# Optimization experiments

Measured on AMD Instinct MI355X. Metric: run time of the kernel, lower is better.

The kernel has to match this reference:

```python
import jax, jax.numpy as jnp
import numpy as np

N = 100000
E = 1600000
H = 2
F_IN = 128
D = 64
DIAL = 256


def setup_inputs() -> dict:
    key = jax.random.key(0)
    ks = jax.random.split(key, 10)
    return {
        "entity_features": jax.random.normal(ks[0], (N, 1, F_IN), jnp.float32),
        "relation_features": jax.random.normal(ks[1], (E, 1, F_IN), jnp.float32),
        "dialogue_context": jax.random.normal(ks[2], (N, DIAL), jnp.float32),
        "w_m": jax.random.normal(ks[3], (H, F_IN, D), jnp.float32) * 0.05,
        "w_q": jax.random.normal(ks[4], (H, F_IN, D), jnp.float32) * 0.05,
        "w_k": jax.random.normal(ks[5], (H, F_IN, D), jnp.float32) * 0.05,
        "w_h_entity": jax.random.normal(ks[6], (H * D, D), jnp.float32) * 0.05,
        "w_h_dialogue": jax.random.normal(ks[7], (DIAL, D), jnp.float32) * 0.05,
        "src": jax.random.randint(ks[8], (E,), 0, N, jnp.int32),
        "dst": jax.random.randint(ks[9], (E,), 0, N, jnp.int32),
    }


def reference(entity_features, relation_features, dialogue_context,
              w_m, w_q, w_k, w_h_entity, w_h_dialogue, src, dst):
    n = entity_features.shape[0]
    h = w_m.shape[0]
    # broadcast single-head features across heads (torch .repeat(1, H, 1))
    f = jnp.broadcast_to(entity_features, (n, h, entity_features.shape[-1]))  # (N,H,F)
    r = jnp.broadcast_to(relation_features,
                         (relation_features.shape[0], h, relation_features.shape[-1]))  # (E,H,F)
    q = jnp.einsum('nhf,hfd->nhd', f, w_q)      # dst attention (N,H,D)
    k = jnp.einsum('nhf,hfd->nhd', f, w_k)      # src attention (N,H,D)
    m = jnp.einsum('nhf,hfd->nhd', f, w_m)      # src message  (N,H,D)
    rm = jnp.einsum('ehf,hfd->ehd', r, w_m)     # edge message (E,H,D)
    # u_dot_v + e_dot_v scores -> (E,H,1)
    q_dst = q[dst]
    e = jnp.sum(k[src] * q_dst, axis=-1, keepdims=True) \
        + jnp.sum(rm * q_dst, axis=-1, keepdims=True)
    e = jnp.where(e >= 0, e, 0.01 * e)  # LeakyReLU(0.01)
    # edge softmax normalized over incoming edges of each dst node, per head
    emax = jax.ops.segment_max(e, dst, num_segments=n)          # (N,H,1)
    ex = jnp.exp(e - emax[dst])
    denom = jax.ops.segment_sum(ex, dst, num_segments=n)        # (N,H,1)
    attn = ex / denom[dst]
    # u_add_e message, weighted, scatter-add to dst
    msg = (m[src] + rm) * attn                                   # (E,H,D)
    agg = jax.ops.segment_sum(msg, dst, num_segments=n)          # (N,H,D)
    rst = agg.reshape(n, -1)                                     # (N,H*D)
    return rst @ w_h_entity + dialogue_context @ w_h_dialogue
```

## Files before the change

kernel.cpp:

```cpp
#include <hip/hip_runtime.h>
#include <hip/hip_bf16.h>
#include <cstdint>


__device__ __forceinline__ unsigned short f2bf(float x) {
    unsigned int u = __float_as_uint(x);
    u += 0x7FFFu + ((u >> 16) & 1u);
    return (unsigned short)(u >> 16);
}
__device__ __forceinline__ float bflo(unsigned int u) { return __uint_as_float(u << 16); }
__device__ __forceinline__ float bfhi(unsigned int u) { return __uint_as_float(u & 0xFFFF0000u); }

__global__ void zero_f4(float4* __restrict__ p, long n4) {
    long i = (long)blockIdx.x * blockDim.x + threadIdx.x;
    long stride = (long)gridDim.x * blockDim.x;
    float4 z = make_float4(0.f, 0.f, 0.f, 0.f);
    for (; i < n4; i += stride) p[i] = z;
}

__global__ void build_w1(const float* __restrict__ wm, const float* __restrict__ wq,
                         const float* __restrict__ wk, float* __restrict__ W1) {
    int idx = blockIdx.x * blockDim.x + threadIdx.x;
    if (idx >= 128 * 640) return;
    int f = idx / 640, c = idx % 640;
    float v;
    if (c < 128) {
        int h = c >> 6, dd = c & 63;
        v = wq[h * 8192 + f * 64 + dd];
    } else if (c < 384) {
        int cc = c - 128, h = cc >> 7, f2 = cc & 127;
        float s = 0.f;
        for (int dd = 0; dd < 64; ++dd)
            s += wq[h * 8192 + f * 64 + dd] * wm[h * 8192 + f2 * 64 + dd];
        v = s;
    } else if (c < 512) {
        int cc = c - 384, h = cc >> 6, dd = cc & 63;
        v = wk[h * 8192 + f * 64 + dd];
    } else {
        int cc = c - 512, h = cc >> 6, dd = cc & 63;
        v = wm[h * 8192 + f * 64 + dd];
    }
    W1[idx] = v;
}

__global__ void build_w2(const float* __restrict__ wm, const float* __restrict__ whe,
                         const float* __restrict__ whd, float* __restrict__ W2) {
    int idx = blockIdx.x * blockDim.x + threadIdx.x;
    if (idx >= 640 * 64) return;
    int rr = idx / 64, j = idx % 64;
    float v;
    if (rr < 128) {
        v = whe[rr * 64 + j];
    } else if (rr < 384) {
        int cc = rr - 128, h = cc >> 7, f2 = cc & 127;
        float s = 0.f;
        for (int dd = 0; dd < 64; ++dd)
            s += wm[h * 8192 + f2 * 64 + dd] * whe[(h * 64 + dd) * 64 + j];
        v = s;
    } else {
        v = whd[(rr - 384) * 64 + j];
    }
    W2[idx] = v;
}

__global__ __launch_bounds__(256) void gemm_proj(
        const float* __restrict__ F, const float* __restrict__ W1,
        unsigned short* __restrict__ Y1, int M) {
    __shared__ float As[128 * 68];
    __shared__ float Bs[128 * 64];
    int m0 = blockIdx.x * 64;
    int bn = blockIdx.y;
    int tid = threadIdx.x;
    #pragma unroll
    for (int i = 0; i < 8; ++i) {
        int s = tid + i * 256;
        int row = s >> 5, cv = s & 31;
        int gr = m0 + row;
        float4 v = make_float4(0.f, 0.f, 0.f, 0.f);
        if (gr < M) v = *(const float4*)(F + (size_t)gr * 128 + cv * 4);
        int k0 = cv * 4;
        As[(k0 + 0) * 68 + row] = v.x;
        As[(k0 + 1) * 68 + row] = v.y;
        As[(k0 + 2) * 68 + row] = v.z;
        As[(k0 + 3) * 68 + row] = v.w;
    }
    #pragma unroll
    for (int i = 0; i < 8; ++i) {
        int s = tid + i * 256;
        int k = s >> 4, cv = s & 15;
        float4 v = *(const float4*)(W1 + (size_t)k * 640 + bn * 64 + cv * 4);
        *(float4*)(Bs + k * 64 + cv * 4) = v;
    }
    __syncthreads();
    int tx = tid & 15, ty = tid >> 4;
    float acc[4][4] = {};
    #pragma unroll 8
    for (int k = 0; k < 128; ++k) {
        float a[4];
        a[0] = As[k * 68 + ty * 4 + 0];
        a[1] = As[k * 68 + ty * 4 + 1];
        a[2] = As[k * 68 + ty * 4 + 2];
        a[3] = As[k * 68 + ty * 4 + 3];
        float4 b = *(const float4*)(Bs + k * 64 + tx * 4);
        #pragma unroll
        for (int i = 0; i < 4; ++i) {
            acc[i][0] += a[i] * b.x;
            acc[i][1] += a[i] * b.y;
            acc[i][2] += a[i] * b.z;
            acc[i][3] += a[i] * b.w;
        }
    }
    #pragma unroll
    for (int i = 0; i < 4; ++i) {
        int gr = m0 + ty * 4 + i;
        if (gr < M) {
            ushort4 st;
            st.x = f2bf(acc[i][0]);
            st.y = f2bf(acc[i][1]);
            st.z = f2bf(acc[i][2]);
            st.w = f2bf(acc[i][3]);
            *(ushort4*)(Y1 + (size_t)gr * 640 + bn * 64 + tx * 4) = st;
        }
    }
}

__global__ void hist_dst(const int* __restrict__ dst, int* __restrict__ cnt, int E) {
    int e = blockIdx.x * blockDim.x + threadIdx.x;
    if (e < E) atomicAdd(&cnt[dst[e]], 1);
}

__global__ void scan_pass1(const int* __restrict__ cnt, int* __restrict__ bsum, int N) {
    __shared__ int sd[256];
    int i = blockIdx.x * 256 + threadIdx.x;
    sd[threadIdx.x] = (i < N) ? cnt[i] : 0;
    __syncthreads();
    for (int s = 128; s > 0; s >>= 1) {
        if (threadIdx.x < s) sd[threadIdx.x] += sd[threadIdx.x + s];
        __syncthreads();
    }
    if (threadIdx.x == 0) bsum[blockIdx.x] = sd[0];
}

__global__ void scan_pass2(int* __restrict__ bsum, int nb) {
    __shared__ int sd[1024];
    int t = threadIdx.x;
    int v = (t < nb) ? bsum[t] : 0;
    sd[t] = v;
    __syncthreads();
    for (int o = 1; o < 1024; o <<= 1) {
        int x = (t >= o) ? sd[t - o] : 0;
        __syncthreads();
        sd[t] += x;
        __syncthreads();
    }
    if (t < nb) bsum[t] = sd[t] - v;
}

__global__ void scan_pass3(const int* __restrict__ cnt, const int* __restrict__ bsum,
                           int* __restrict__ off, int* __restrict__ cursor, int N, int E) {
    __shared__ int sd[256];
    int t = threadIdx.x;
    int i = blockIdx.x * 256 + t;
    int v = (i < N) ? cnt[i] : 0;
    sd[t] = v;
    __syncthreads();
    for (int o = 1; o < 256; o <<= 1) {
        int x = (t >= o) ? sd[t - o] : 0;
        __syncthreads();
        sd[t] += x;
        __syncthreads();
    }
    int excl = sd[t] - v + bsum[blockIdx.x];
    if (i < N) { off[i] = excl; cursor[i] = excl; }
    if (i == N - 1) off[N] = E;
}

__global__ void scatter_edges(const int* __restrict__ dst, int* __restrict__ cursor,
                              int* __restrict__ elist, int E) {
    int e = blockIdx.x * blockDim.x + threadIdx.x;
    if (e < E) {
        int p = atomicAdd(&cursor[dst[e]], 1);
        elist[p] = e;
    }
}

__global__ __launch_bounds__(256) void node_gather(
        const float* __restrict__ R, const int* __restrict__ srcArr,
        const int* __restrict__ off, const int* __restrict__ elist,
        const unsigned short* __restrict__ Y1,
        float* __restrict__ Xagg, float* __restrict__ denom, int N) {
    int n = blockIdx.x * 4 + (threadIdx.x >> 6);
    if (n >= N) return;
    int l = threadIdx.x & 63;
    const unsigned int* yd = (const unsigned int*)(Y1 + (size_t)n * 640);
    unsigned int qu = yd[l], t0u = yd[64 + l], t1u = yd[128 + l];
    float qx = bflo(qu),  qy = bfhi(qu);
    float t0x = bflo(t0u), t0y = bfhi(t0u);
    float t1x = bflo(t1u), t1y = bfhi(t1u);
    int e0 = off[n], e1 = off[n + 1];
    float maccx = 0.f, maccy = 0.f;
    float s0x = 0.f, s0y = 0.f, s1x = 0.f, s1y = 0.f;
    float den0 = 0.f, den1 = 0.f;
    for (int e = e0; e < e1; ++e) {
        int eid = elist[e];
        int sI = srcArr[eid];
        const unsigned int* ys = (const unsigned int*)(Y1 + (size_t)sI * 640);
        unsigned int ku = ys[192 + l];
        unsigned int mu = ys[256 + l];
        float2 rv = *(const float2*)(R + (size_t)eid * 128 + 2 * l);
        float kx = bflo(ku), ky = bfhi(ku);
        float mx = bflo(mu), my = bfhi(mu);
        float kqp = kx * qx + ky * qy;
        float a0 = rv.x * t0x + rv.y * t0y;
        float a1 = rv.x * t1x + rv.y * t1y;
        if (l < 32) a0 += kqp; else a1 += kqp;
        #pragma unroll
        for (int o = 32; o; o >>= 1) {
            a0 += __shfl_xor(a0, o);
            a1 += __shfl_xor(a1, o);
        }
        a0 = (a0 >= 0.f) ? a0 : 0.01f * a0;
        a1 = (a1 >= 0.f) ? a1 : 0.01f * a1;
        float p0 = __expf(a0), p1 = __expf(a1);
        float w = (l < 32) ? p0 : p1;
        maccx += w * mx;  maccy += w * my;
        s0x += p0 * rv.x; s0y += p0 * rv.y;
        s1x += p1 * rv.x; s1y += p1 * rv.y;
        den0 += p0; den1 += p1;
    }
    float* xd = Xagg + (size_t)n * 384;
    *(float2*)(xd + 2 * l)       = make_float2(maccx, maccy);
    *(float2*)(xd + 128 + 2 * l) = make_float2(s0x, s0y);
    *(float2*)(xd + 256 + 2 * l) = make_float2(s1x, s1y);
    if (l == 0) {
        denom[(size_t)n * 2]     = den0;
        denom[(size_t)n * 2 + 1] = den1;
    }
}

__global__ __launch_bounds__(256) void gemm_out(
        const float* __restrict__ Xagg, const float* __restrict__ denom,
        const float* __restrict__ dial, const float* __restrict__ W2,
        float* __restrict__ out, int M) {
    __shared__ float Xs[64 * 68];
    __shared__ float Ws[64 * 64];
    int m0 = blockIdx.x * 64;
    int tid = threadIdx.x;
    int tx = tid & 15, ty = tid >> 4;
    float acc[4][4] = {};
    for (int kc = 0; kc < 10; ++kc) {
        #pragma unroll
        for (int i = 0; i < 4; ++i) {
            int s = tid + i * 256;
            int row = s >> 4, cv = s & 15;
            int gr = m0 + row;
            int c0 = kc * 64 + cv * 4;
            float4 v = make_float4(0.f, 0.f, 0.f, 0.f);
            if (gr < M) {
                if (c0 < 384) {
                    v = *(const float4*)(Xagg + (size_t)gr * 384 + c0);
                    int h = (c0 < 128) ? (c0 >> 6) : ((c0 - 128) >> 7);
                    float den = denom[(size_t)gr * 2 + h];
                    float sc = (den > 0.f) ? (1.f / den) : 0.f;
                    v.x *= sc; v.y *= sc; v.z *= sc; v.w *= sc;
                } else {
                    v = *(const float4*)(dial + (size_t)gr * 256 + (c0 - 384));
                }
            }
            int k0 = cv * 4;
            Xs[(k0 + 0) * 68 + row] = v.x;
            Xs[(k0 + 1) * 68 + row] = v.y;
            Xs[(k0 + 2) * 68 + row] = v.z;
            Xs[(k0 + 3) * 68 + row] = v.w;
        }
        #pragma unroll
        for (int i = 0; i < 4; ++i) {
            int s = tid + i * 256;
            int k = s >> 4, cv = s & 15;
            *(float4*)(Ws + k * 64 + cv * 4) =
                *(const float4*)(W2 + (size_t)(kc * 64 + k) * 64 + cv * 4);
        }
        __syncthreads();
        #pragma unroll 8
        for (int k = 0; k < 64; ++k) {
            float a[4];
            a[0] = Xs[k * 68 + ty * 4 + 0];
            a[1] = Xs[k * 68 + ty * 4 + 1];
            a[2] = Xs[k * 68 + ty * 4 + 2];
            a[3] = Xs[k * 68 + ty * 4 + 3];
            float4 b = *(const float4*)(Ws + k * 64 + tx * 4);
            #pragma unroll
            for (int i = 0; i < 4; ++i) {
                acc[i][0] += a[i] * b.x;
                acc[i][1] += a[i] * b.y;
                acc[i][2] += a[i] * b.z;
                acc[i][3] += a[i] * b.w;
            }
        }
        __syncthreads();
    }
    #pragma unroll
    for (int i = 0; i < 4; ++i) {
        int gr = m0 + ty * 4 + i;
        if (gr < M) {
            float4 st = make_float4(acc[i][0], acc[i][1], acc[i][2], acc[i][3]);
            *(float4*)(out + (size_t)gr * 64 + tx * 4) = st;
        }
    }
}

extern "C" void kernel_launch(void* const* d_in, const int* in_sizes, int n_in,
                              void* d_out, int out_size, void* d_ws, size_t ws_size,
                              hipStream_t stream) {
    const float* entity = (const float*)d_in[0];
    const float* rel    = (const float*)d_in[1];
    const float* dial   = (const float*)d_in[2];
    const float* wm     = (const float*)d_in[3];
    const float* wq     = (const float*)d_in[4];
    const float* wk     = (const float*)d_in[5];
    const float* whe    = (const float*)d_in[6];
    const float* whd    = (const float*)d_in[7];
    const int*   src    = (const int*)d_in[8];
    const int*   dst    = (const int*)d_in[9];
    int N = in_sizes[0] / 128;
    int E = in_sizes[8];
    float* out = (float*)d_out;

    float* ws    = (float*)d_ws;
    float* Xagg  = ws;
    float* denom = Xagg + (size_t)N * 384;
    float* W1    = denom + (size_t)N * 2;
    float* W2    = W1 + 128 * 640;
    unsigned short* Y1 = (unsigned short*)(W2 + 640 * 64);
    int* ip      = (int*)(Y1 + (size_t)N * 640);
    int* cnt     = ip;
    int* offp    = cnt + N;
    int* cursor  = offp + N + 1;
    int* elist   = cursor + N;
    int* bsum    = elist + E;

    int nb = (N + 255) / 256;

    zero_f4<<<256, 256, 0, stream>>>((float4*)cnt, (long)N / 4);
    build_w1<<<(128 * 640 + 255) / 256, 256, 0, stream>>>(wm, wq, wk, W1);
    build_w2<<<(640 * 64 + 255) / 256, 256, 0, stream>>>(wm, whe, whd, W2);
    dim3 g1((N + 63) / 64, 10);
    gemm_proj<<<g1, 256, 0, stream>>>(entity, W1, Y1, N);
    hist_dst<<<(E + 255) / 256, 256, 0, stream>>>(dst, cnt, E);
    scan_pass1<<<nb, 256, 0, stream>>>(cnt, bsum, N);
    scan_pass2<<<1, 1024, 0, stream>>>(bsum, nb);
    scan_pass3<<<nb, 256, 0, stream>>>(cnt, bsum, offp, cursor, N, E);
    scatter_edges<<<(E + 255) / 256, 256, 0, stream>>>(dst, cursor, elist, E);
    node_gather<<<(N + 3) / 4, 256, 0, stream>>>(rel, src, offp, elist, Y1, Xagg, denom, N);
    gemm_out<<<(N + 63) / 64, 256, 0, stream>>>(Xagg, denom, dial, W2, out, N);
}
```

Baseline: 2.005 ms.

## Use bf16x3 split MFMA for projection and output GEMMs

Replaces the two fp32 SIMT GEMMs with MFMA 16x16x32 bf16 kernels that emulate fp32 precision by splitting operands into high and low bf16 parts (three MFMAs per tile). Weight matrices are prebuilt transposed and split into hi/lo buffers, and tiles grow to 128 rows. The aim is to cut the ALU cost of the dense projections, at the price of more LDS, split conversion work and narrower output stores.

```diff
diff --git a/kernel.cpp b/kernel.cpp
--- a/kernel.cpp
+++ b/kernel.cpp
@@ -2,6 +2,9 @@
 #include <hip/hip_bf16.h>
 #include <cstdint>
 
+
+typedef __attribute__((ext_vector_type(8))) short bf16x8;
+typedef __attribute__((ext_vector_type(4))) float f32x4;
 
 __device__ __forceinline__ unsigned short f2bf(float x) {
     unsigned int u = __float_as_uint(x);
@@ -10,6 +13,13 @@
 }
 __device__ __forceinline__ float bflo(unsigned int u) { return __uint_as_float(u << 16); }
 __device__ __forceinline__ float bfhi(unsigned int u) { return __uint_as_float(u & 0xFFFF0000u); }
+
+__device__ __forceinline__ void splitbf(float x, unsigned short& h, unsigned short& l) {
+    unsigned short hh = f2bf(x);
+    float rem = x - __uint_as_float((unsigned int)hh << 16);
+    h = hh;
+    l = f2bf(rem);
+}
 
 __global__ void zero_f4(float4* __restrict__ p, long n4) {
     long i = (long)blockIdx.x * blockDim.x + threadIdx.x;
@@ -19,7 +29,9 @@
 }
 
 __global__ void build_w1(const float* __restrict__ wm, const float* __restrict__ wq,
-                         const float* __restrict__ wk, float* __restrict__ W1) {
+                         const float* __restrict__ wk,
+                         unsigned short* __restrict__ W1tH,
+                         unsigned short* __restrict__ W1tL) {
     int idx = blockIdx.x * blockDim.x + threadIdx.x;
     if (idx >= 128 * 640) return;
     int f = idx / 640, c = idx % 640;
@@ -40,11 +52,16 @@
         int cc = c - 512, h = cc >> 6, dd = cc & 63;
         v = wm[h * 8192 + f * 64 + dd];
     }
-    W1[idx] = v;
+    unsigned short h16, l16;
+    splitbf(v, h16, l16);
+    W1tH[(size_t)c * 128 + f] = h16;
+    W1tL[(size_t)c * 128 + f] = l16;
 }
 
 __global__ void build_w2(const float* __restrict__ wm, const float* __restrict__ whe,
-                         const float* __restrict__ whd, float* __restrict__ W2) {
+                         const float* __restrict__ whd,
+                         unsigned short* __restrict__ W2tH,
+                         unsigned short* __restrict__ W2tL) {
     int idx = blockIdx.x * blockDim.x + threadIdx.x;
     if (idx >= 640 * 64) return;
     int rr = idx / 64, j = idx % 64;
@@ -60,66 +77,93 @@
     } else {
         v = whd[(rr - 384) * 64 + j];
     }
-    W2[idx] = v;
-}
-
-__global__ __launch_bounds__(256) void gemm_proj(
-        const float* __restrict__ F, const float* __restrict__ W1,
+    unsigned short h16, l16;
+    splitbf(v, h16, l16);
+    W2tH[(size_t)j * 640 + rr] = h16;
+    W2tL[(size_t)j * 640 + rr] = l16;
+}
+
+__global__ __launch_bounds__(256) void gemm_proj_mfma(
+        const float* __restrict__ F,
+        const unsigned short* __restrict__ W1tH, const unsigned short* __restrict__ W1tL,
         unsigned short* __restrict__ Y1, int M) {
-    __shared__ float As[128 * 68];
-    __shared__ float Bs[128 * 64];
-    int m0 = blockIdx.x * 64;
-    int bn = blockIdx.y;
+    __shared__ unsigned short AH[128 * 136];
+    __shared__ unsigned short AL[128 * 136];
+    __shared__ unsigned short BH[128 * 136];
+    __shared__ unsigned short BL[128 * 136];
+    int m0 = blockIdx.x * 128;
+    int n0 = blockIdx.y * 128;
     int tid = threadIdx.x;
+
+    {
+        int row = tid >> 1, seg = tid & 1;
+        int gr = m0 + row;
+        const float* src = F + (size_t)gr * 128 + seg * 64;
+        unsigned short* dh = AH + row * 136 + seg * 64;
+        unsigned short* dl = AL + row * 136 + seg * 64;
+        #pragma unroll
+        for (int v = 0; v < 16; ++v) {
+            float4 x = make_float4(0.f, 0.f, 0.f, 0.f);
+            if (gr < M) x = *(const float4*)(src + v * 4);
+            ushort4 h4, l4;
+            splitbf(x.x, h4.x, l4.x);
+            splitbf(x.y, h4.y, l4.y);
+            splitbf(x.z, h4.z, l4.z);
+            splitbf(x.w, h4.w, l4.w);
+            *(ushort4*)(dh + v * 4) = h4;
+            *(ushort4*)(dl + v * 4) = l4;
+        }
+    }
+    {
+        int row = tid >> 1, seg = tid & 1;
+        const unsigned short* sh = W1tH + (size_t)(n0 + row) * 128 + seg * 64;
+        const unsigned short* sl = W1tL + (size_t)(n0 + row) * 128 + seg * 64;
+        unsigned short* dh = BH + row * 136 + seg * 64;
+        unsigned short* dl = BL + row * 136 + seg * 64;
+        #pragma unroll
+        for (int v = 0; v < 8; ++v) {
+            *(uint4*)(dh + v * 8) = *(const uint4*)(sh + v * 8);
+            *(uint4*)(dl + v * 8) = *(const uint4*)(sl + v * 8);
+        }
+    }
+    __syncthreads();
+
+    int l = tid & 63, wid = tid >> 6;
+    int wr = (wid >> 1) * 64, wc = (wid & 1) * 64;
+    int r16 = l & 15, k8 = (l >> 4) * 8;
+    f32x4 acc[4][4] = {};
     #pragma unroll
-    for (int i = 0; i < 8; ++i) {
-        int s = tid + i * 256;
-        int row = s >> 5, cv = s & 31;
-        int gr = m0 + row;
-        float4 v = make_float4(0.f, 0.f, 0.f, 0.f);
-        if (gr < M) v = *(const float4*)(F + (size_t)gr * 128 + cv * 4);
-        int k0 = cv * 4;
-        As[(k0 + 0) * 68 + row] = v.x;
-        As[(k0 + 1) * 68 + row] = v.y;
-        As[(k0 + 2) * 68 + row] = v.z;
-        As[(k0 + 3) * 68 + row] = v.w;
-    }
-    #pragma unroll
-    for (int i = 0; i < 8; ++i) {
-        int s = tid + i * 256;
-        int k = s >> 4, cv = s & 15;
-        float4 v = *(const float4*)(W1 + (size_t)k * 640 + bn * 64 + cv * 4);
-        *(float4*)(Bs + k * 64 + cv * 4) = v;
-    }
-    __syncthreads();
-    int tx = tid & 15, ty = tid >> 4;
-    float acc[4][4] = {};
-    #pragma unroll 8
-    for (int k = 0; k < 128; ++k) {
-        float a[4];
-        a[0] = As[k * 68 + ty * 4 + 0];
-        a[1] = As[k * 68 + ty * 4 + 1];
-        a[2] = As[k * 68 + ty * 4 + 2];
-        a[3] = As[k * 68 + ty * 4 + 3];
-        float4 b = *(const float4*)(Bs + k * 64 + tx * 4);
+    for (int kc = 0; kc < 4; ++kc) {
+        int ko = kc * 32 + k8;
+        bf16x8 ah[4], al[4], bh[4], bl[4];
         #pragma unroll
         for (int i = 0; i < 4; ++i) {
-            acc[i][0] += a[i] * b.x;
-            acc[i][1] += a[i] * b.y;
-            acc[i][2] += a[i] * b.z;
-            acc[i][3] += a[i] * b.w;
-        }
-    }
+            ah[i] = *(const bf16x8*)(AH + (wr + i * 16 + r16) * 136 + ko);
+            al[i] = *(const bf16x8*)(AL + (wr + i * 16 + r16) * 136 + ko);
+            bh[i] = *(const bf16x8*)(BH + (wc + i * 16 + r16) * 136 + ko);
+            bl[i] = *(const bf16x8*)(BL + (wc + i * 16 + r16) * 136 + ko);
+        }
+        #pragma unroll
+        for (int i = 0; i < 4; ++i) {
+            #pragma unroll
+            for (int j = 0; j < 4; ++j) {
+                acc[i][j] = __builtin_amdgcn_mfma_f32_16x16x32_bf16(ah[i], bh[j], acc[i][j], 0, 0, 0);
+                acc[i][j] = __builtin_amdgcn_mfma_f32_16x16x32_bf16(ah[i], bl[j], acc[i][j], 0, 0, 0);
+                acc[i][j] = __builtin_amdgcn_mfma_f32_16x16x32_bf16(al[i], bh[j], acc[i][j], 0, 0, 0);
+            }
+        }
+    }
+    int g4 = (l >> 4) * 4, c16 = l & 15;
     #pragma unroll
     for (int i = 0; i < 4; ++i) {
-        int gr = m0 + ty * 4 + i;
-        if (gr < M) {
-            ushort4 st;
-            st.x = f2bf(acc[i][0]);
-            st.y = f2bf(acc[i][1]);
-            st.z = f2bf(acc[i][2]);
-            st.w = f2bf(acc[i][3]);
-            *(ushort4*)(Y1 + (size_t)gr * 640 + bn * 64 + tx * 4) = st;
+        #pragma unroll
+        for (int r = 0; r < 4; ++r) {
+            int gr = m0 + wr + i * 16 + g4 + r;
+            if (gr < M) {
+                #pragma unroll
+                for (int j = 0; j < 4; ++j)
+                    Y1[(size_t)gr * 640 + n0 + wc + j * 16 + c16] = f2bf(acc[i][j][r]);
+            }
         }
     }
 }
@@ -238,73 +282,109 @@
     }
 }
 
-__global__ __launch_bounds__(256) void gemm_out(
+__global__ __launch_bounds__(256) void gemm_out_mfma(
         const float* __restrict__ Xagg, const float* __restrict__ denom,
-        const float* __restrict__ dial, const float* __restrict__ W2,
+        const float* __restrict__ dial,
+        const unsigned short* __restrict__ W2tH, const unsigned short* __restrict__ W2tL,
         float* __restrict__ out, int M) {
-    __shared__ float Xs[64 * 68];
-    __shared__ float Ws[64 * 64];
-    int m0 = blockIdx.x * 64;
+    __shared__ unsigned short XH[128 * 136];
+    __shared__ unsigned short XL[128 * 136];
+    __shared__ unsigned short WH[64 * 136];
+    __shared__ unsigned short WL[64 * 136];
+    int m0 = blockIdx.x * 128;
     int tid = threadIdx.x;
-    int tx = tid & 15, ty = tid >> 4;
-    float acc[4][4] = {};
-    for (int kc = 0; kc < 10; ++kc) {
-        #pragma unroll
-        for (int i = 0; i < 4; ++i) {
-            int s = tid + i * 256;
-            int row = s >> 4, cv = s & 15;
-            int gr = m0 + row;
-            int c0 = kc * 64 + cv * 4;
-            float4 v = make_float4(0.f, 0.f, 0.f, 0.f);
-            if (gr < M) {
-                if (c0 < 384) {
-                    v = *(const float4*)(Xagg + (size_t)gr * 384 + c0);
-                    int h = (c0 < 128) ? (c0 >> 6) : ((c0 - 128) >> 7);
-                    float den = denom[(size_t)gr * 2 + h];
-                    float sc = (den > 0.f) ? (1.f / den) : 0.f;
-                    v.x *= sc; v.y *= sc; v.z *= sc; v.w *= sc;
-                } else {
-                    v = *(const float4*)(dial + (size_t)gr * 256 + (c0 - 384));
+    int l = tid & 63, wid = tid >> 6;
+    int wr = (wid >> 1) * 64, wc = (wid & 1) * 32;
+    int r16 = l & 15, k8 = (l >> 4) * 8;
+    f32x4 acc[4][2] = {};
+
+    int row = tid >> 1, seg = tid & 1;
+    int gr = m0 + row;
+    float sc0 = 0.f, sc1 = 0.f;
+    if (gr < M) {
+        float d0 = denom[(size_t)gr * 2], d1 = denom[(size_t)gr * 2 + 1];
+        sc0 = (d0 > 0.f) ? 1.f / d0 : 0.f;
+        sc1 = (d1 > 0.f) ? 1.f / d1 : 0.f;
+    }
+
+    for (int kc = 0; kc < 5; ++kc) {
+        {
+            int c0 = kc * 128 + seg * 64;
+            unsigned short* dh = XH + row * 136 + seg * 64;
+            unsigned short* dl = XL + row * 136 + seg * 64;
+            #pragma unroll
+            for (int v = 0; v < 16; ++v) {
+                int cc = c0 + v * 4;
+                float4 x = make_float4(0.f, 0.f, 0.f, 0.f);
+                if (gr < M) {
+                    if (cc < 384) {
+                        x = *(const float4*)(Xagg + (size_t)gr * 384 + cc);
+                        float s = (cc < 128) ? ((cc & 64) ? sc1 : sc0)
+                                             : ((cc < 256) ? sc0 : sc1);
+                        x.x *= s; x.y *= s; x.z *= s; x.w *= s;
+                    } else {
+                        x = *(const float4*)(dial + (size_t)gr * 256 + (cc - 384));
+                    }
                 }
-            }
-            int k0 = cv * 4;
-            Xs[(k0 + 0) * 68 + row] = v.x;
-            Xs[(k0 + 1) * 68 + row] = v.y;
-            Xs[(k0 + 2) * 68 + row] = v.z;
-            Xs[(k0 + 3) * 68 + row] = v.w;
-        }
-        #pragma unroll
-        for (int i = 0; i < 4; ++i) {
-            int s = tid + i * 256;
-            int k = s >> 4, cv = s & 15;
-            *(float4*)(Ws + k * 64 + cv * 4) =
-                *(const float4*)(W2 + (size_t)(kc * 64 + k) * 64 + cv * 4);
-        }
-        __syncthreads();
-        #pragma unroll 8
-        for (int k = 0; k < 64; ++k) {
-            float a[4];
-            a[0] = Xs[k * 68 + ty * 4 + 0];
-            a[1] = Xs[k * 68 + ty * 4 + 1];
-            a[2] = Xs[k * 68 + ty * 4 + 2];
-            a[3] = Xs[k * 68 + ty * 4 + 3];
-            float4 b = *(const float4*)(Ws + k * 64 + tx * 4);
+                ushort4 h4, l4;
+                splitbf(x.x, h4.x, l4.x);
+                splitbf(x.y, h4.y, l4.y);
+                splitbf(x.z, h4.z, l4.z);
+                splitbf(x.w, h4.w, l4.w);
+                *(ushort4*)(dh + v * 4) = h4;
+                *(ushort4*)(dl + v * 4) = l4;
+            }
+        }
+        {
+            int n = tid >> 2, s4 = tid & 3;
+            const unsigned short* sh = W2tH + (size_t)n * 640 + kc * 128 + s4 * 32;
+            const unsigned short* sl = W2tL + (size_t)n * 640 + kc * 128 + s4 * 32;
+            unsigned short* dh = WH + n * 136 + s4 * 32;
+            unsigned short* dl = WL + n * 136 + s4 * 32;
+            #pragma unroll
+            for (int v = 0; v < 4; ++v) {
+                *(uint4*)(dh + v * 8) = *(const uint4*)(sh + v * 8);
+                *(uint4*)(dl + v * 8) = *(const uint4*)(sl + v * 8);
+            }
+        }
+        __syncthreads();
+        #pragma unroll
+        for (int k2 = 0; k2 < 4; ++k2) {
+            int ko = k2 * 32 + k8;
+            bf16x8 ah[4], al[4], bh[2], bl[2];
             #pragma unroll
             for (int i = 0; i < 4; ++i) {
-                acc[i][0] += a[i] * b.x;
-                acc[i][1] += a[i] * b.y;
-                acc[i][2] += a[i] * b.z;
-                acc[i][3] += a[i] * b.w;
-            }
-        }
-        __syncthreads();
-    }
+                ah[i] = *(const bf16x8*)(XH + (wr + i * 16 + r16) * 136 + ko);
+                al[i] = *(const bf16x8*)(XL + (wr + i * 16 + r16) * 136 + ko);
+            }
+            #pragma unroll
+            for (int j = 0; j < 2; ++j) {
+                bh[j] = *(const bf16x8*)(WH + (wc + j * 16 + r16) * 136 + ko);
+                bl[j] = *(const bf16x8*)(WL + (wc + j * 16 + r16) * 136 + ko);
+            }
+            #pragma unroll
+            for (int i = 0; i < 4; ++i) {
+                #pragma unroll
+                for (int j = 0; j < 2; ++j) {
+                    acc[i][j] = __builtin_amdgcn_mfma_f32_16x16x32_bf16(ah[i], bh[j], acc[i][j], 0, 0, 0);
+                    acc[i][j] = __builtin_amdgcn_mfma_f32_16x16x32_bf16(ah[i], bl[j], acc[i][j], 0, 0, 0);
+                    acc[i][j] = __builtin_amdgcn_mfma_f32_16x16x32_bf16(al[i], bh[j], acc[i][j], 0, 0, 0);
+                }
+            }
+        }
+        __syncthreads();
+    }
+    int g4 = (l >> 4) * 4, c16 = l & 15;
     #pragma unroll
     for (int i = 0; i < 4; ++i) {
-        int gr = m0 + ty * 4 + i;
-        if (gr < M) {
-            float4 st = make_float4(acc[i][0], acc[i][1], acc[i][2], acc[i][3]);
-            *(float4*)(out + (size_t)gr * 64 + tx * 4) = st;
+        #pragma unroll
+        for (int r = 0; r < 4; ++r) {
+            int gr2 = m0 + wr + i * 16 + g4 + r;
+            if (gr2 < M) {
+                #pragma unroll
+                for (int j = 0; j < 2; ++j)
+                    out[(size_t)gr2 * 64 + wc + j * 16 + c16] = acc[i][j][r];
+            }
         }
     }
 }
@@ -329,10 +409,12 @@
     float* ws    = (float*)d_ws;
     float* Xagg  = ws;
     float* denom = Xagg + (size_t)N * 384;
-    float* W1    = denom + (size_t)N * 2;
-    float* W2    = W1 + 128 * 640;
-    unsigned short* Y1 = (unsigned short*)(W2 + 640 * 64);
-    int* ip      = (int*)(Y1 + (size_t)N * 640);
+    unsigned short* Y1   = (unsigned short*)(denom + (size_t)N * 2);
+    unsigned short* W1tH = Y1 + (size_t)N * 640;
+    unsigned short* W1tL = W1tH + 640 * 128;
+    unsigned short* W2tH = W1tL + 640 * 128;
+    unsigned short* W2tL = W2tH + 64 * 640;
+    int* ip      = (int*)(W2tL + 64 * 640);
     int* cnt     = ip;
     int* offp    = cnt + N;
     int* cursor  = offp + N + 1;
@@ -342,15 +424,15 @@
     int nb = (N + 255) / 256;
 
     zero_f4<<<256, 256, 0, stream>>>((float4*)cnt, (long)N / 4);
-    build_w1<<<(128 * 640 + 255) / 256, 256, 0, stream>>>(wm, wq, wk, W1);
-    build_w2<<<(640 * 64 + 255) / 256, 256, 0, stream>>>(wm, whe, whd, W2);
-    dim3 g1((N + 63) / 64, 10);
-    gemm_proj<<<g1, 256, 0, stream>>>(entity, W1, Y1, N);
+    build_w1<<<(128 * 640 + 255) / 256, 256, 0, stream>>>(wm, wq, wk, W1tH, W1tL);
+    build_w2<<<(640 * 64 + 255) / 256, 256, 0, stream>>>(wm, whe, whd, W2tH, W2tL);
+    dim3 g1((N + 127) / 128, 5);
+    gemm_proj_mfma<<<g1, 256, 0, stream>>>(entity, W1tH, W1tL, Y1, N);
     hist_dst<<<(E + 255) / 256, 256, 0, stream>>>(dst, cnt, E);
     scan_pass1<<<nb, 256, 0, stream>>>(cnt, bsum, N);
     scan_pass2<<<1, 1024, 0, stream>>>(bsum, nb);
     scan_pass3<<<nb, 256, 0, stream>>>(cnt, bsum, offp, cursor, N, E);
     scatter_edges<<<(E + 255) / 256, 256, 0, stream>>>(dst, cursor, elist, E);
     node_gather<<<(N + 3) / 4, 256, 0, stream>>>(rel, src, offp, elist, Y1, Xagg, denom, N);
-    gemm_out<<<(N + 63) / 64, 256, 0, stream>>>(Xagg, denom, dial, W2, out, N);
-}
+    gemm_out_mfma<<<(N + 127) / 128, 256, 0, stream>>>(Xagg, denom, dial, W2tH, W2tL, out, N);
+}
```

Result: faster. 1.877 ms (-6.4%).
